# Kernel optimization log

Hardware: AMD Instinct MI355X
Metric: run time of the kernel (lower is better)

## Reference

```python
import jax, jax.numpy as jnp
import numpy as np

N = 50000      # nodes
E = 800000     # edges (before self-loops)
H = 2          # attention heads
C = 64         # hidden_channels (per-head out since concat=False)
L = 3          # num_layers - 2 conv blocks
OUT = 128      # readout out_channels
G = 512        # num graphs
VOCAB = 100    # embedding table size
NEG_SLOPE = 0.2


def setup_inputs() -> dict:
    key = jax.random.key(0)
    ks = jax.random.split(key, 12)
    s = 1.0 / np.sqrt(C)
    x = jax.random.randint(ks[0], (N,), 0, VOCAB, dtype=jnp.int32)
    edge_index = jax.random.randint(ks[1], (2, E), 0, N, dtype=jnp.int32)
    batch = jnp.sort(jax.random.randint(ks[2], (N,), 0, G, dtype=jnp.int32))
    embed = jax.random.normal(ks[3], (VOCAB, C), dtype=jnp.float32) * s
    lin_W = jax.random.normal(ks[4], (L, C, C), dtype=jnp.float32) * s
    lin_b = jnp.zeros((L, C), dtype=jnp.float32)
    gat_Wl = jax.random.normal(ks[5], (L, C, H * C), dtype=jnp.float32) * s
    gat_bl = jnp.zeros((L, H * C), dtype=jnp.float32)
    gat_Wr = jax.random.normal(ks[6], (L, C, H * C), dtype=jnp.float32) * s
    gat_br = jnp.zeros((L, H * C), dtype=jnp.float32)
    gat_att = jax.random.normal(ks[7], (L, H, C), dtype=jnp.float32) * s
    gat_bias = jnp.zeros((L, C), dtype=jnp.float32)
    readout_W = jax.random.normal(ks[8], (C, OUT), dtype=jnp.float32) * s
    readout_b = jnp.zeros((OUT,), dtype=jnp.float32)
    return {"x": x, "edge_index": edge_index, "batch": batch, "num_graphs": G,
            "embed": embed, "lin_W": lin_W, "lin_b": lin_b,
            "gat_Wl": gat_Wl, "gat_bl": gat_bl, "gat_Wr": gat_Wr, "gat_br": gat_br,
            "gat_att": gat_att, "gat_bias": gat_bias,
            "readout_W": readout_W, "readout_b": readout_b}


def _gatv2_layer(h, src, dst, Wl, bl, Wr, br, att, bias):
    # lin_l -> source/message features, lin_r -> target features (PyG GATv2Conv)
    xl = (h @ Wl + bl).reshape(N, H, C)
    xr = (h @ Wr + br).reshape(N, H, C)
    # per-edge GATv2 score: a^T LeakyReLU(x_l[j] + x_r[i])
    e = jax.nn.leaky_relu(xl[src] + xr[dst], NEG_SLOPE)      # [E2,H,C]
    score = jnp.einsum('ehc,hc->eh', e, att)                 # [E2,H]
    # segment softmax over incoming edges of each dst node (stable)
    m = jax.lax.stop_gradient(jax.ops.segment_max(score, dst, num_segments=N))
    p = jnp.exp(score - m[dst])
    denom = jax.ops.segment_sum(p, dst, num_segments=N)      # [N,H]
    alpha = p / denom[dst]                                   # [E2,H]
    msg = xl[src] * alpha[:, :, None]                        # [E2,H,C]
    agg = jax.ops.segment_sum(msg, dst, num_segments=N)      # [N,H,C]
    return agg.mean(axis=1) + bias                           # concat=False -> head mean


def reference(x, edge_index, batch, num_graphs, embed, lin_W, lin_b,
              gat_Wl, gat_bl, gat_Wr, gat_br, gat_att, gat_bias,
              readout_W, readout_b):
    # add self loops (GATv2Conv default add_self_loops=True)
    loops = jnp.arange(N, dtype=edge_index.dtype)
    src = jnp.concatenate([edge_index[0], loops])
    dst = jnp.concatenate([edge_index[1], loops])
    h = embed[x]                                             # [N,C]
    for l in range(L):
        h = jax.nn.relu(h @ lin_W[l] + lin_b[l])             # dropout is a no-op in eval
        h = _gatv2_layer(h, src, dst, gat_Wl[l], gat_bl[l], gat_Wr[l], gat_br[l],
                         gat_att[l], gat_bias[l])
    out = h @ readout_W + readout_b                          # [N,OUT]
    return jax.ops.segment_sum(out, batch, num_segments=num_graphs)  # [G,OUT]
```

## Files before the change

### kernel.cpp

```cpp
#include <hip/hip_runtime.h>
#include <hip/hip_fp16.h>

#define N_NODES  50000
#define E_EDGES  800000
#define E_TOT    850000
#define H_HEADS  2
#define C_DIM    64
#define HC       128
#define L_LAYERS 3
#define OUT_DIM  128
#define G_GRAPHS 512
#define NEG_SLOPE 0.2f
#define NB       196
#define EPB      4096

typedef float v2f __attribute__((ext_vector_type(2)));

__device__ __forceinline__ void lds_fence() { asm volatile("" ::: "memory"); }

__global__ void init_kernel(float* __restrict__ out, int* __restrict__ bucket_counts) {
    int i = blockIdx.x * 256 + threadIdx.x;
    if (i < G_GRAPHS * OUT_DIM) out[i] = 0.f;
    if (blockIdx.x == 0) bucket_counts[threadIdx.x] = 0;
}

__global__ void bucket_count_kernel(const int* __restrict__ dsts, int* __restrict__ bucket_counts) {
    __shared__ int hist[256];
    int tid = threadIdx.x;
    hist[tid] = 0;
    __syncthreads();
    int ebase = blockIdx.x * EPB;
#pragma unroll
    for (int i = 0; i < 16; i++) {
        int e = ebase + i * 256 + tid;
        if (e < E_TOT) {
            int d = (e < E_EDGES) ? dsts[e] : e - E_EDGES;
            atomicAdd(&hist[d >> 8], 1);
        }
    }
    __syncthreads();
    if (hist[tid]) atomicAdd(&bucket_counts[tid], hist[tid]);
}

__global__ void scan196_kernel(const int* __restrict__ bucket_counts,
                               int* __restrict__ bwptr, int* __restrict__ bbase) {
    __shared__ int wsum[4];
    int tid = threadIdx.x;
    int lane = tid & 63, wid = tid >> 6;
    int cnt = (tid < NB) ? bucket_counts[tid] : 0;
    int v = cnt;
#pragma unroll
    for (int off = 1; off < 64; off <<= 1) {
        int t = __shfl_up(v, off, 64);
        if (lane >= off) v += t;
    }
    if (lane == 63) wsum[wid] = v;
    __syncthreads();
    int woff = 0;
#pragma unroll
    for (int w = 0; w < 4; w++) if (w < wid) woff += wsum[w];
    v += woff;
    if (tid < NB) { bwptr[tid] = v - cnt; bbase[tid] = v - cnt; }
    if (tid == 0) bbase[NB] = E_TOT;
}

__global__ void edge_partition_kernel(const int* __restrict__ srcs, const int* __restrict__ dsts,
                                      int* __restrict__ bwptr, unsigned int* __restrict__ ebuf) {
    __shared__ int hist[256];
    __shared__ int lscan[256];
    __shared__ int sExcl[256];
    __shared__ int lcnt[256];
    __shared__ int gbase[256];
    __shared__ unsigned int sval[EPB];
    __shared__ unsigned char sgid[EPB];
    int tid = threadIdx.x;
    int ebase = blockIdx.x * EPB;
    hist[tid] = 0;
    __syncthreads();
    unsigned int val[16];
    int gid[16];
#pragma unroll
    for (int i = 0; i < 16; i++) {
        int e = ebase + i * 256 + tid;
        if (e < E_TOT) {
            int s, d;
            if (e < E_EDGES) { s = srcs[e]; d = dsts[e]; }
            else             { s = d = e - E_EDGES; }
            val[i] = ((unsigned)s << 8) | (unsigned)(d & 255);
            gid[i] = d >> 8;
            atomicAdd(&hist[gid[i]], 1);
        } else gid[i] = -1;
    }
    __syncthreads();
    lscan[tid] = hist[tid];
    __syncthreads();
#pragma unroll
    for (int off = 1; off < 256; off <<= 1) {
        int t = (tid >= off) ? lscan[tid - off] : 0;
        __syncthreads();
        lscan[tid] += t;
        __syncthreads();
    }
    sExcl[tid] = lscan[tid] - hist[tid];
    lcnt[tid] = 0;
    __syncthreads();
#pragma unroll
    for (int i = 0; i < 16; i++) {
        if (gid[i] >= 0) {
            int off = atomicAdd(&lcnt[gid[i]], 1);
            int idx = sExcl[gid[i]] + off;
            sval[idx] = val[i];
            sgid[idx] = (unsigned char)gid[i];
        }
    }
    if (tid < NB) {
        int c = hist[tid];
        gbase[tid] = c ? atomicAdd(&bwptr[tid], c) : 0;
    }
    __syncthreads();
    int total = lscan[255];
    for (int idx = tid; idx < total; idx += 256) {
        int g = sgid[idx];
        ebuf[gbase[g] + (idx - sExcl[g])] = sval[idx];
    }
}

__global__ void bucket_csr_kernel(const unsigned int* __restrict__ ebuf,
                                  const int* __restrict__ bbase,
                                  int* __restrict__ row_ptr,
                                  unsigned short* __restrict__ src_sorted) {
    __shared__ int hist[256];
    __shared__ int lcnt[256];
    __shared__ int wsum[4];
    int g = blockIdx.x, tid = threadIdx.x;
    int n0 = g << 8;
    int nodes = min(256, N_NODES - n0);
    int b0 = bbase[g], b1 = bbase[g + 1];
    int cnt = b1 - b0;
    hist[tid] = 0;
    lcnt[tid] = 0;
    __syncthreads();
    for (int i = tid; i < cnt; i += 256) atomicAdd(&hist[ebuf[b0 + i] & 255], 1);
    __syncthreads();
    int c = hist[tid];
    int v = c;
    int lane = tid & 63, wid = tid >> 6;
#pragma unroll
    for (int off = 1; off < 64; off <<= 1) {
        int t = __shfl_up(v, off, 64);
        if (lane >= off) v += t;
    }
    if (lane == 63) wsum[wid] = v;
    __syncthreads();
    int woff = 0;
#pragma unroll
    for (int w = 0; w < 4; w++) if (w < wid) woff += wsum[w];
    v += woff;
    int nbase = b0 + v - c;
    if (tid < nodes) row_ptr[n0 + tid] = nbase;
    if (g == NB - 1 && tid == 0) row_ptr[N_NODES] = E_TOT;
    __syncthreads();
    hist[tid] = nbase;
    __syncthreads();
    for (int i = tid; i < cnt; i += 256) {
        unsigned int e = ebuf[b0 + i];
        int dl = e & 255;
        int slot = hist[dl] + atomicAdd(&lcnt[dl], 1);
        src_sorted[slot] = (unsigned short)(e >> 8);
    }
}

__global__ void layer_lin_kernel(const float* __restrict__ h,
                                 const int* __restrict__ xs, const float* __restrict__ etab,
                                 int use_embed,
                                 const float* __restrict__ W, const float* __restrict__ b,
                                 const float* __restrict__ Wl, const float* __restrict__ bl,
                                 const float* __restrict__ Wr, const float* __restrict__ br,
                                 __half* __restrict__ xlh, float* __restrict__ xri) {
    __shared__ float sH[16 * 64];
    __shared__ float sH2[16 * 64];
    int tid = threadIdx.x;
    int base = blockIdx.x * 16;
#pragma unroll
    for (int i = 0; i < 4; i++) {
        int idx = tid + i * 256;
        int nn = base + (idx >> 6);
        int cc = idx & 63;
        float hv = 0.f;
        if (nn < N_NODES)
            hv = use_embed ? etab[xs[nn] * 64 + cc] : h[(size_t)nn * 64 + cc];
        sH[idx] = hv;
    }
    __syncthreads();
    {
        int c = tid & 63, g = tid >> 6;
        float a0 = b[c], a1 = a0, a2 = a0, a3 = a0;
        for (int k = 0; k < 64; k++) {
            float wv = W[k * 64 + c];
            a0 = fmaf(sH[(g * 4 + 0) * 64 + k], wv, a0);
            a1 = fmaf(sH[(g * 4 + 1) * 64 + k], wv, a1);
            a2 = fmaf(sH[(g * 4 + 2) * 64 + k], wv, a2);
            a3 = fmaf(sH[(g * 4 + 3) * 64 + k], wv, a3);
        }
        sH2[(g * 4 + 0) * 64 + c] = fmaxf(a0, 0.f);
        sH2[(g * 4 + 1) * 64 + c] = fmaxf(a1, 0.f);
        sH2[(g * 4 + 2) * 64 + c] = fmaxf(a2, 0.f);
        sH2[(g * 4 + 3) * 64 + c] = fmaxf(a3, 0.f);
    }
    __syncthreads();
    {
        int j = tid & 127, gg = tid >> 7;
        float accl[8], accr[8];
#pragma unroll
        for (int n = 0; n < 8; n++) { accl[n] = bl[j]; accr[n] = br[j]; }
        for (int k = 0; k < 64; k++) {
            float wl = Wl[k * 128 + j], wr = Wr[k * 128 + j];
#pragma unroll
            for (int n = 0; n < 8; n++) {
                float hv = sH2[(gg * 8 + n) * 64 + k];
                accl[n] = fmaf(hv, wl, accl[n]);
                accr[n] = fmaf(hv, wr, accr[n]);
            }
        }
        int hh = j >> 6, c = j & 63;
#pragma unroll
        for (int n = 0; n < 8; n++) {
            int node = base + gg * 8 + n;
            if (node < N_NODES) {
                size_t o = (size_t)node * 128 + c * 2 + hh;
                xlh[o] = __float2half(accl[n]);
                xri[o] = accr[n];
            }
        }
    }
}

__global__ void gat_kernel(const __half2* __restrict__ xlh, const float2* __restrict__ xr2,
                           const float* __restrict__ att, const int* __restrict__ row_ptr,
                           const unsigned short* __restrict__ src_sorted,
                           const float* __restrict__ bias,
                           float* __restrict__ h_out) {
    __shared__ __align__(16) float cbuf[4][8 * 132];
    int w = threadIdx.x >> 6;
    int d = blockIdx.x * 4 + w;
    if (d >= N_NODES) return;
    int lane = threadIdx.x & 63;
    int r0 = row_ptr[d], r1 = row_ptr[d + 1];
    float2 vrf = xr2[(size_t)d * 64 + lane];
    v2f vr2 = {vrf.x, vrf.y};
    v2f att2 = {att[lane], att[64 + lane]};
    float* cb = cbuf[w];
    int e_of = lane >> 3, p = lane & 7;

    float dpx = 0.f, dpy = 0.f;
    v2f ac0 = {0.f, 0.f}, ac1 = {0.f, 0.f};

#define GAT_LOAD(V, CB) do {                                                    \
        int lim_ = nchunk - 1;                                                  \
        _Pragma("unroll")                                                       \
        for (int e = 0; e < 8; e++) {                                           \
            int ee_ = (CB) + e;                                                 \
            int sv_ = __builtin_amdgcn_readlane(idx, (ee_ < nchunk) ? ee_ : lim_); \
            V[e] = xlh[(size_t)sv_ * 64 + lane];                                \
        }                                                                       \
    } while (0)

#define GAT_PROC(V, CB) do {                                                    \
        int rem_ = nchunk - (CB);                                               \
        v2f vf8[8];                                                             \
        _Pragma("unroll")                                                       \
        for (int e = 0; e < 8; e++) {                                           \
            float2 vf_ = __half22float2(V[e]);                                  \
            v2f vl2 = {vf_.x, vf_.y};                                           \
            vf8[e] = vl2;                                                       \
            v2f z = vl2 + vr2;                                                  \
            v2f t = __builtin_elementwise_max(z, z * NEG_SLOPE) * att2;         \
            *(v2f*)&cb[e * 132 + 2 * lane] = t;                                 \
        }                                                                       \
        lds_fence();                                                            \
        v2f s2 = {0.f, 0.f};                                                    \
        {                                                                       \
            const float4* row_ = (const float4*)&cb[e_of * 132 + p * 16];       \
            _Pragma("unroll")                                                   \
            for (int j = 0; j < 4; j++) {                                       \
                float4 f = row_[j];                                             \
                s2 += (v2f){f.x, f.y};                                          \
                s2 += (v2f){f.z, f.w};                                          \
            }                                                                   \
        }                                                                       \
        lds_fence();                                                            \
        _Pragma("unroll")                                                       \
        for (int off = 1; off <= 4; off <<= 1) {                                \
            v2f o_;                                                             \
            o_.x = __shfl_xor(s2.x, off, 64);                                   \
            o_.y = __shfl_xor(s2.y, off, 64);                                   \
            s2 += o_;                                                           \
        }                                                                       \
        float sx = s2.x, sy = s2.y;                                             \
        if (e_of >= rem_) { sx = -INFINITY; sy = -INFINITY; }                   \
        float wx = __expf(sx), wy = __expf(sy);                                 \
        dpx += wx; dpy += wy;                                                   \
        _Pragma("unroll")                                                       \
        for (int e = 0; e < 8; e++) {                                           \
            float swx = __int_as_float(__builtin_amdgcn_readlane(__float_as_int(wx), 8 * e)); \
            float swy = __int_as_float(__builtin_amdgcn_readlane(__float_as_int(wy), 8 * e)); \
            v2f w2 = {swx, swy};                                                \
            if (e & 1) ac1 = __builtin_elementwise_fma(w2, vf8[e], ac1);        \
            else       ac0 = __builtin_elementwise_fma(w2, vf8[e], ac0);        \
        }                                                                       \
    } while (0)

    for (int base = r0; base < r1; base += 64) {
        int a = base + lane;
        int idx = (int)src_sorted[(a < r1) ? a : (r1 - 1)];
        int nchunk = min(64, r1 - base);
        __half2 va[8], vb[8];
        GAT_LOAD(va, 0);
        int cb_i = 0;
        for (;;) {
            int nx = cb_i + 8;
            if (nx < nchunk) {
                GAT_LOAD(vb, nx);
                GAT_PROC(va, cb_i);
                cb_i = nx;
            } else {
                GAT_PROC(va, cb_i);
                break;
            }
            nx = cb_i + 8;
            if (nx < nchunk) {
                GAT_LOAD(va, nx);
                GAT_PROC(vb, cb_i);
                cb_i = nx;
            } else {
                GAT_PROC(vb, cb_i);
                break;
            }
        }
    }
#undef GAT_LOAD
#undef GAT_PROC

#pragma unroll
    for (int off = 8; off <= 32; off <<= 1) {
        dpx += __shfl_xor(dpx, off, 64);
        dpy += __shfl_xor(dpy, off, 64);
    }
    v2f acc = ac0 + ac1;
    h_out[(size_t)d * 64 + lane] = (acc.x / dpx + acc.y / dpy) * 0.5f + bias[lane];
}

__global__ void readout_kernel(const float* __restrict__ h, const float* __restrict__ W,
                               const float* __restrict__ b, const int* __restrict__ batch,
                               float* __restrict__ out) {
    __shared__ float sH[16 * 64];
    __shared__ int sB[16];
    int tid = threadIdx.x;
    int base = blockIdx.x * 16;
#pragma unroll
    for (int i = 0; i < 4; i++) {
        int idx = tid + i * 256;
        int nn = base + (idx >> 6);
        sH[idx] = (nn < N_NODES) ? h[(size_t)nn * 64 + (idx & 63)] : 0.f;
    }
    if (tid < 16) sB[tid] = (base + tid < N_NODES) ? batch[base + tid] : -1;
    __syncthreads();
    int j = tid & 127, gg = tid >> 7;
    float acc[8];
#pragma unroll
    for (int n = 0; n < 8; n++) acc[n] = b[j];
    for (int k = 0; k < 64; k++) {
        float wv = W[k * OUT_DIM + j];
#pragma unroll
        for (int n = 0; n < 8; n++) acc[n] = fmaf(sH[(gg * 8 + n) * 64 + k], wv, acc[n]);
    }
    float run = 0.f; int curb = -2;
#pragma unroll
    for (int n = 0; n < 8; n++) {
        int node = base + gg * 8 + n;
        int bb = (node < N_NODES) ? sB[gg * 8 + n] : -1;
        if (bb != curb) {
            if (curb >= 0) atomicAdd(&out[curb * OUT_DIM + j], run);
            run = 0.f; curb = bb;
        }
        if (bb >= 0) run += acc[n];
    }
    if (curb >= 0) atomicAdd(&out[curb * OUT_DIM + j], run);
}

extern "C" void kernel_launch(void* const* d_in, const int* in_sizes, int n_in,
                              void* d_out, int out_size, void* d_ws, size_t ws_size,
                              hipStream_t stream) {
    const int*   x        = (const int*)d_in[0];
    const int*   edge     = (const int*)d_in[1];
    const int*   batch    = (const int*)d_in[2];
    const float* embed    = (const float*)d_in[4];
    const float* lin_W    = (const float*)d_in[5];
    const float* lin_b    = (const float*)d_in[6];
    const float* gat_Wl   = (const float*)d_in[7];
    const float* gat_bl   = (const float*)d_in[8];
    const float* gat_Wr   = (const float*)d_in[9];
    const float* gat_br   = (const float*)d_in[10];
    const float* gat_att  = (const float*)d_in[11];
    const float* gat_bias = (const float*)d_in[12];
    const float* ro_W     = (const float*)d_in[13];
    const float* ro_b     = (const float*)d_in[14];
    float* out = (float*)d_out;

    const int* srcs = edge;
    const int* dsts = edge + E_EDGES;

    float* h    = (float*)d_ws;
    __half* xlh = (__half*)(h + (size_t)N_NODES * 64);
    float* xr   = (float*)((char*)xlh + (size_t)N_NODES * HC * sizeof(__half));
    int* row_ptr       = (int*)(xr + (size_t)N_NODES * HC);
    int* bwptr         = row_ptr + N_NODES + 1;
    int* bbase         = bwptr + 256;
    int* bucket_counts = bbase + 256;
    unsigned int* ebuf = (unsigned int*)(bucket_counts + 256);
    unsigned short* src_sorted = (unsigned short*)(ebuf + E_TOT);

    const int T = 256;
    const int gInit = (G_GRAPHS * OUT_DIM + 255) / 256;
    const int gPart = (E_TOT + EPB - 1) / EPB;
    const int gLin  = (N_NODES + 15) / 16;
    const int gGat  = (N_NODES + 3) / 4;

    init_kernel<<<gInit, T, 0, stream>>>(out, bucket_counts);
    bucket_count_kernel<<<gPart, T, 0, stream>>>(dsts, bucket_counts);
    scan196_kernel<<<1, T, 0, stream>>>(bucket_counts, bwptr, bbase);
    edge_partition_kernel<<<gPart, T, 0, stream>>>(srcs, dsts, bwptr, ebuf);
    bucket_csr_kernel<<<NB, T, 0, stream>>>(ebuf, bbase, row_ptr, src_sorted);

    for (int l = 0; l < L_LAYERS; l++) {
        layer_lin_kernel<<<gLin, T, 0, stream>>>(
            h, x, embed, (l == 0) ? 1 : 0,
            lin_W + (size_t)l * 64 * 64, lin_b + (size_t)l * 64,
            gat_Wl + (size_t)l * 64 * 128, gat_bl + (size_t)l * 128,
            gat_Wr + (size_t)l * 64 * 128, gat_br + (size_t)l * 128,
            xlh, xr);
        gat_kernel<<<gGat, T, 0, stream>>>(
            (const __half2*)xlh, (const float2*)xr, gat_att + (size_t)l * HC,
            row_ptr, src_sorted, gat_bias + (size_t)l * 64, h);
    }

    readout_kernel<<<gLin, T, 0, stream>>>(h, ro_W, ro_b, batch, out);
}
```

Measured before the change: 407.8 us.

## Store xr in fp16, transpose LDS tiles with packed FMA, shrink GAT blocks

Three separate changes. xr is now stored as fp16 instead of fp32, which halves its write and read traffic. The linear and readout kernels now keep transposed LDS tiles, so float4 LDS reads feed packed v2f FMAs. The GAT kernel runs 128-thread blocks (two waves) instead of 256, which is meant to give finer scheduling granularity. The fp16 xr lowers precision of the attention score inputs.

```diff
diff --git a/kernel.cpp b/kernel.cpp
--- a/kernel.cpp
+++ b/kernel.cpp
@@ -176,9 +176,9 @@
                                  const float* __restrict__ W, const float* __restrict__ b,
                                  const float* __restrict__ Wl, const float* __restrict__ bl,
                                  const float* __restrict__ Wr, const float* __restrict__ br,
-                                 __half* __restrict__ xlh, float* __restrict__ xri) {
-    __shared__ float sH[16 * 64];
-    __shared__ float sH2[16 * 64];
+                                 __half* __restrict__ xlh, __half* __restrict__ xrh) {
+    __shared__ float sHT[64 * 16];
+    __shared__ float sH2T[64 * 16];
     int tid = threadIdx.x;
     int base = blockIdx.x * 16;
 #pragma unroll
@@ -189,64 +189,75 @@
         float hv = 0.f;
         if (nn < N_NODES)
             hv = use_embed ? etab[xs[nn] * 64 + cc] : h[(size_t)nn * 64 + cc];
-        sH[idx] = hv;
+        sHT[cc * 16 + (idx >> 6)] = hv;
     }
     __syncthreads();
     {
         int c = tid & 63, g = tid >> 6;
-        float a0 = b[c], a1 = a0, a2 = a0, a3 = a0;
+        v2f a01 = {b[c], b[c]}, a23 = a01;
         for (int k = 0; k < 64; k++) {
             float wv = W[k * 64 + c];
-            a0 = fmaf(sH[(g * 4 + 0) * 64 + k], wv, a0);
-            a1 = fmaf(sH[(g * 4 + 1) * 64 + k], wv, a1);
-            a2 = fmaf(sH[(g * 4 + 2) * 64 + k], wv, a2);
-            a3 = fmaf(sH[(g * 4 + 3) * 64 + k], wv, a3);
-        }
-        sH2[(g * 4 + 0) * 64 + c] = fmaxf(a0, 0.f);
-        sH2[(g * 4 + 1) * 64 + c] = fmaxf(a1, 0.f);
-        sH2[(g * 4 + 2) * 64 + c] = fmaxf(a2, 0.f);
-        sH2[(g * 4 + 3) * 64 + c] = fmaxf(a3, 0.f);
+            v2f w2 = {wv, wv};
+            float4 hA = *(const float4*)&sHT[k * 16 + g * 4];
+            a01 = __builtin_elementwise_fma((v2f){hA.x, hA.y}, w2, a01);
+            a23 = __builtin_elementwise_fma((v2f){hA.z, hA.w}, w2, a23);
+        }
+        float4 r;
+        r.x = fmaxf(a01.x, 0.f); r.y = fmaxf(a01.y, 0.f);
+        r.z = fmaxf(a23.x, 0.f); r.w = fmaxf(a23.y, 0.f);
+        *(float4*)&sH2T[c * 16 + g * 4] = r;
     }
     __syncthreads();
     {
         int j = tid & 127, gg = tid >> 7;
-        float accl[8], accr[8];
-#pragma unroll
-        for (int n = 0; n < 8; n++) { accl[n] = bl[j]; accr[n] = br[j]; }
+        v2f accl2[4], accr2[4];
+#pragma unroll
+        for (int m = 0; m < 4; m++) { accl2[m] = (v2f){bl[j], bl[j]}; accr2[m] = (v2f){br[j], br[j]}; }
         for (int k = 0; k < 64; k++) {
             float wl = Wl[k * 128 + j], wr = Wr[k * 128 + j];
-#pragma unroll
-            for (int n = 0; n < 8; n++) {
-                float hv = sH2[(gg * 8 + n) * 64 + k];
-                accl[n] = fmaf(hv, wl, accl[n]);
-                accr[n] = fmaf(hv, wr, accr[n]);
+            v2f wl2 = {wl, wl}, wr2 = {wr, wr};
+            float4 hA = *(const float4*)&sH2T[k * 16 + gg * 8];
+            float4 hB = *(const float4*)&sH2T[k * 16 + gg * 8 + 4];
+            accl2[0] = __builtin_elementwise_fma((v2f){hA.x, hA.y}, wl2, accl2[0]);
+            accl2[1] = __builtin_elementwise_fma((v2f){hA.z, hA.w}, wl2, accl2[1]);
+            accl2[2] = __builtin_elementwise_fma((v2f){hB.x, hB.y}, wl2, accl2[2]);
+            accl2[3] = __builtin_elementwise_fma((v2f){hB.z, hB.w}, wl2, accl2[3]);
+            accr2[0] = __builtin_elementwise_fma((v2f){hA.x, hA.y}, wr2, accr2[0]);
+            accr2[1] = __builtin_elementwise_fma((v2f){hA.z, hA.w}, wr2, accr2[1]);
+            accr2[2] = __builtin_elementwise_fma((v2f){hB.x, hB.y}, wr2, accr2[2]);
+            accr2[3] = __builtin_elementwise_fma((v2f){hB.z, hB.w}, wr2, accr2[3]);
+        }
+        int hh = j >> 6, c = j & 63;
+#pragma unroll
+        for (int m = 0; m < 4; m++) {
+#pragma unroll
+            for (int s = 0; s < 2; s++) {
+                int node = base + gg * 8 + 2 * m + s;
+                if (node < N_NODES) {
+                    size_t o = (size_t)node * 128 + c * 2 + hh;
+                    float vl = s ? accl2[m].y : accl2[m].x;
+                    float vr = s ? accr2[m].y : accr2[m].x;
+                    xlh[o] = __float2half(vl);
+                    xrh[o] = __float2half(vr);
+                }
             }
         }
-        int hh = j >> 6, c = j & 63;
-#pragma unroll
-        for (int n = 0; n < 8; n++) {
-            int node = base + gg * 8 + n;
-            if (node < N_NODES) {
-                size_t o = (size_t)node * 128 + c * 2 + hh;
-                xlh[o] = __float2half(accl[n]);
-                xri[o] = accr[n];
-            }
-        }
-    }
-}
-
-__global__ void gat_kernel(const __half2* __restrict__ xlh, const float2* __restrict__ xr2,
-                           const float* __restrict__ att, const int* __restrict__ row_ptr,
-                           const unsigned short* __restrict__ src_sorted,
-                           const float* __restrict__ bias,
-                           float* __restrict__ h_out) {
-    __shared__ __align__(16) float cbuf[4][8 * 132];
+    }
+}
+
+__global__ void __launch_bounds__(128)
+gat_kernel(const __half2* __restrict__ xlh, const __half2* __restrict__ xrh2,
+           const float* __restrict__ att, const int* __restrict__ row_ptr,
+           const unsigned short* __restrict__ src_sorted,
+           const float* __restrict__ bias,
+           float* __restrict__ h_out) {
+    __shared__ __align__(16) float cbuf[2][8 * 132];
     int w = threadIdx.x >> 6;
-    int d = blockIdx.x * 4 + w;
+    int d = blockIdx.x * 2 + w;
     if (d >= N_NODES) return;
     int lane = threadIdx.x & 63;
     int r0 = row_ptr[d], r1 = row_ptr[d + 1];
-    float2 vrf = xr2[(size_t)d * 64 + lane];
+    float2 vrf = __half22float2(xrh2[(size_t)d * 64 + lane]);
     v2f vr2 = {vrf.x, vrf.y};
     v2f att2 = {att[lane], att[64 + lane]};
     float* cb = cbuf[w];
@@ -353,7 +364,7 @@
 __global__ void readout_kernel(const float* __restrict__ h, const float* __restrict__ W,
                                const float* __restrict__ b, const int* __restrict__ batch,
                                float* __restrict__ out) {
-    __shared__ float sH[16 * 64];
+    __shared__ float sHT[64 * 16];
     __shared__ int sB[16];
     int tid = threadIdx.x;
     int base = blockIdx.x * 16;
@@ -361,29 +372,36 @@
     for (int i = 0; i < 4; i++) {
         int idx = tid + i * 256;
         int nn = base + (idx >> 6);
-        sH[idx] = (nn < N_NODES) ? h[(size_t)nn * 64 + (idx & 63)] : 0.f;
+        float hv = (nn < N_NODES) ? h[(size_t)nn * 64 + (idx & 63)] : 0.f;
+        sHT[(idx & 63) * 16 + (idx >> 6)] = hv;
     }
     if (tid < 16) sB[tid] = (base + tid < N_NODES) ? batch[base + tid] : -1;
     __syncthreads();
     int j = tid & 127, gg = tid >> 7;
-    float acc[8];
-#pragma unroll
-    for (int n = 0; n < 8; n++) acc[n] = b[j];
+    v2f acc2[4];
+#pragma unroll
+    for (int m = 0; m < 4; m++) acc2[m] = (v2f){b[j], b[j]};
     for (int k = 0; k < 64; k++) {
         float wv = W[k * OUT_DIM + j];
-#pragma unroll
-        for (int n = 0; n < 8; n++) acc[n] = fmaf(sH[(gg * 8 + n) * 64 + k], wv, acc[n]);
+        v2f w2 = {wv, wv};
+        float4 hA = *(const float4*)&sHT[k * 16 + gg * 8];
+        float4 hB = *(const float4*)&sHT[k * 16 + gg * 8 + 4];
+        acc2[0] = __builtin_elementwise_fma((v2f){hA.x, hA.y}, w2, acc2[0]);
+        acc2[1] = __builtin_elementwise_fma((v2f){hA.z, hA.w}, w2, acc2[1]);
+        acc2[2] = __builtin_elementwise_fma((v2f){hB.x, hB.y}, w2, acc2[2]);
+        acc2[3] = __builtin_elementwise_fma((v2f){hB.z, hB.w}, w2, acc2[3]);
     }
     float run = 0.f; int curb = -2;
 #pragma unroll
     for (int n = 0; n < 8; n++) {
         int node = base + gg * 8 + n;
         int bb = (node < N_NODES) ? sB[gg * 8 + n] : -1;
+        float av = (n & 1) ? acc2[n >> 1].y : acc2[n >> 1].x;
         if (bb != curb) {
             if (curb >= 0) atomicAdd(&out[curb * OUT_DIM + j], run);
             run = 0.f; curb = bb;
         }
-        if (bb >= 0) run += acc[n];
+        if (bb >= 0) run += av;
     }
     if (curb >= 0) atomicAdd(&out[curb * OUT_DIM + j], run);
 }
@@ -412,8 +430,8 @@
 
     float* h    = (float*)d_ws;
     __half* xlh = (__half*)(h + (size_t)N_NODES * 64);
-    float* xr   = (float*)((char*)xlh + (size_t)N_NODES * HC * sizeof(__half));
-    int* row_ptr       = (int*)(xr + (size_t)N_NODES * HC);
+    __half* xrh = xlh + (size_t)N_NODES * HC;
+    int* row_ptr       = (int*)(xrh + (size_t)N_NODES * HC);
     int* bwptr         = row_ptr + N_NODES + 1;
     int* bbase         = bwptr + 256;
     int* bucket_counts = bbase + 256;
@@ -424,7 +442,7 @@
     const int gInit = (G_GRAPHS * OUT_DIM + 255) / 256;
     const int gPart = (E_TOT + EPB - 1) / EPB;
     const int gLin  = (N_NODES + 15) / 16;
-    const int gGat  = (N_NODES + 3) / 4;
+    const int gGat  = (N_NODES + 1) / 2;
 
     init_kernel<<<gInit, T, 0, stream>>>(out, bucket_counts);
     bucket_count_kernel<<<gPart, T, 0, stream>>>(dsts, bucket_counts);
@@ -438,9 +456,9 @@
             lin_W + (size_t)l * 64 * 64, lin_b + (size_t)l * 64,
             gat_Wl + (size_t)l * 64 * 128, gat_bl + (size_t)l * 128,
             gat_Wr + (size_t)l * 64 * 128, gat_br + (size_t)l * 128,
-            xlh, xr);
-        gat_kernel<<<gGat, T, 0, stream>>>(
-            (const __half2*)xlh, (const float2*)xr, gat_att + (size_t)l * HC,
+            xlh, xrh);
+        gat_kernel<<<gGat, 128, 0, stream>>>(
+            (const __half2*)xlh, (const __half2*)xrh, gat_att + (size_t)l * HC,
             row_ptr, src_sorted, gat_bias + (size_t)l * 64, h);
     }
 
```

Result: slower. 1.491 ms (+265.6%).

## Fuse CSR build into cooperative kernel, store xr in fp16, shrink GAT blocks

Applied to the files above, without the earlier changes.

Folds the five CSR-construction kernels (init, bucket count, scan, partition, per-bucket CSR) into one cooperative kernel on 256 blocks, separated by grid-wide syncs, to cut launch overhead and inter-kernel gaps. The target-side projection xr is now stored as fp16 instead of fp32, halving its write and read traffic in the linear and GAT kernels. The GAT kernel moves from 256-thread to 128-thread blocks (two destination nodes per block) for finer scheduling. Risks are the cost of grid.sync and fewer blocks during CSR build, plus reduced precision in the attention logits.

```diff
diff --git a/kernel.cpp b/kernel.cpp
--- a/kernel.cpp
+++ b/kernel.cpp
@@ -1,5 +1,8 @@
 #include <hip/hip_runtime.h>
 #include <hip/hip_fp16.h>
+#include <hip/hip_cooperative_groups.h>
+
+namespace cg = cooperative_groups;
 
 #define N_NODES  50000
 #define E_EDGES  800000
@@ -13,59 +16,19 @@
 #define NEG_SLOPE 0.2f
 #define NB       196
 #define EPB      4096
+#define NCHUNK   ((E_TOT + EPB - 1) / EPB)
 
 typedef float v2f __attribute__((ext_vector_type(2)));
 
 __device__ __forceinline__ void lds_fence() { asm volatile("" ::: "memory"); }
 
-__global__ void init_kernel(float* __restrict__ out, int* __restrict__ bucket_counts) {
-    int i = blockIdx.x * 256 + threadIdx.x;
-    if (i < G_GRAPHS * OUT_DIM) out[i] = 0.f;
-    if (blockIdx.x == 0) bucket_counts[threadIdx.x] = 0;
-}
-
-__global__ void bucket_count_kernel(const int* __restrict__ dsts, int* __restrict__ bucket_counts) {
-    __shared__ int hist[256];
-    int tid = threadIdx.x;
-    hist[tid] = 0;
-    __syncthreads();
-    int ebase = blockIdx.x * EPB;
-#pragma unroll
-    for (int i = 0; i < 16; i++) {
-        int e = ebase + i * 256 + tid;
-        if (e < E_TOT) {
-            int d = (e < E_EDGES) ? dsts[e] : e - E_EDGES;
-            atomicAdd(&hist[d >> 8], 1);
-        }
-    }
-    __syncthreads();
-    if (hist[tid]) atomicAdd(&bucket_counts[tid], hist[tid]);
-}
-
-__global__ void scan196_kernel(const int* __restrict__ bucket_counts,
-                               int* __restrict__ bwptr, int* __restrict__ bbase) {
-    __shared__ int wsum[4];
-    int tid = threadIdx.x;
-    int lane = tid & 63, wid = tid >> 6;
-    int cnt = (tid < NB) ? bucket_counts[tid] : 0;
-    int v = cnt;
-#pragma unroll
-    for (int off = 1; off < 64; off <<= 1) {
-        int t = __shfl_up(v, off, 64);
-        if (lane >= off) v += t;
-    }
-    if (lane == 63) wsum[wid] = v;
-    __syncthreads();
-    int woff = 0;
-#pragma unroll
-    for (int w = 0; w < 4; w++) if (w < wid) woff += wsum[w];
-    v += woff;
-    if (tid < NB) { bwptr[tid] = v - cnt; bbase[tid] = v - cnt; }
-    if (tid == 0) bbase[NB] = E_TOT;
-}
-
-__global__ void edge_partition_kernel(const int* __restrict__ srcs, const int* __restrict__ dsts,
-                                      int* __restrict__ bwptr, unsigned int* __restrict__ ebuf) {
+__global__ void __launch_bounds__(256)
+csr_fused_kernel(const int* __restrict__ srcs, const int* __restrict__ dsts,
+                 float* __restrict__ out, int* __restrict__ bucket_counts,
+                 int* __restrict__ bwptr, int* __restrict__ bbase,
+                 int* __restrict__ row_ptr, unsigned int* __restrict__ ebuf,
+                 unsigned short* __restrict__ src_sorted) {
+    cg::grid_group grid = cg::this_grid();
     __shared__ int hist[256];
     __shared__ int lscan[256];
     __shared__ int sExcl[256];
@@ -74,99 +37,142 @@
     __shared__ unsigned int sval[EPB];
     __shared__ unsigned char sgid[EPB];
     int tid = threadIdx.x;
-    int ebase = blockIdx.x * EPB;
-    hist[tid] = 0;
-    __syncthreads();
-    unsigned int val[16];
-    int gid[16];
-#pragma unroll
-    for (int i = 0; i < 16; i++) {
-        int e = ebase + i * 256 + tid;
-        if (e < E_TOT) {
-            int s, d;
-            if (e < E_EDGES) { s = srcs[e]; d = dsts[e]; }
-            else             { s = d = e - E_EDGES; }
-            val[i] = ((unsigned)s << 8) | (unsigned)(d & 255);
-            gid[i] = d >> 8;
-            atomicAdd(&hist[gid[i]], 1);
-        } else gid[i] = -1;
-    }
-    __syncthreads();
-    lscan[tid] = hist[tid];
-    __syncthreads();
-#pragma unroll
-    for (int off = 1; off < 256; off <<= 1) {
-        int t = (tid >= off) ? lscan[tid - off] : 0;
-        __syncthreads();
-        lscan[tid] += t;
-        __syncthreads();
-    }
-    sExcl[tid] = lscan[tid] - hist[tid];
-    lcnt[tid] = 0;
-    __syncthreads();
-#pragma unroll
-    for (int i = 0; i < 16; i++) {
-        if (gid[i] >= 0) {
-            int off = atomicAdd(&lcnt[gid[i]], 1);
-            int idx = sExcl[gid[i]] + off;
-            sval[idx] = val[i];
-            sgid[idx] = (unsigned char)gid[i];
-        }
-    }
-    if (tid < NB) {
+    int bid = blockIdx.x;
+    int nb = gridDim.x;
+
+    for (int i = bid * 256 + tid; i < G_GRAPHS * OUT_DIM; i += nb * 256) out[i] = 0.f;
+    if (bid == 0) bucket_counts[tid] = 0;
+    grid.sync();
+
+    for (int c = bid; c < NCHUNK; c += nb) {
+        hist[tid] = 0;
+        __syncthreads();
+        int ebase = c * EPB;
+#pragma unroll
+        for (int i = 0; i < 16; i++) {
+            int e = ebase + i * 256 + tid;
+            if (e < E_TOT) {
+                int d = (e < E_EDGES) ? dsts[e] : e - E_EDGES;
+                atomicAdd(&hist[d >> 8], 1);
+            }
+        }
+        __syncthreads();
+        if (hist[tid]) atomicAdd(&bucket_counts[tid], hist[tid]);
+        __syncthreads();
+    }
+    grid.sync();
+
+    if (bid == 0) {
+        int lane = tid & 63, wid = tid >> 6;
+        int cnt = (tid < NB) ? bucket_counts[tid] : 0;
+        int v = cnt;
+#pragma unroll
+        for (int off = 1; off < 64; off <<= 1) {
+            int t = __shfl_up(v, off, 64);
+            if (lane >= off) v += t;
+        }
+        if (lane == 63) gbase[wid] = v;
+        __syncthreads();
+        int woff = 0;
+#pragma unroll
+        for (int w = 0; w < 4; w++) if (w < wid) woff += gbase[w];
+        v += woff;
+        if (tid < NB) { bwptr[tid] = v - cnt; bbase[tid] = v - cnt; }
+        if (tid == 0) bbase[NB] = E_TOT;
+    }
+    grid.sync();
+
+    for (int c = bid; c < NCHUNK; c += nb) {
+        int ebase = c * EPB;
+        hist[tid] = 0;
+        __syncthreads();
+        unsigned int val[16];
+        int gid[16];
+#pragma unroll
+        for (int i = 0; i < 16; i++) {
+            int e = ebase + i * 256 + tid;
+            if (e < E_TOT) {
+                int s, d;
+                if (e < E_EDGES) { s = srcs[e]; d = dsts[e]; }
+                else             { s = d = e - E_EDGES; }
+                val[i] = ((unsigned)s << 8) | (unsigned)(d & 255);
+                gid[i] = d >> 8;
+                atomicAdd(&hist[gid[i]], 1);
+            } else gid[i] = -1;
+        }
+        __syncthreads();
+        lscan[tid] = hist[tid];
+        __syncthreads();
+#pragma unroll
+        for (int off = 1; off < 256; off <<= 1) {
+            int t = (tid >= off) ? lscan[tid - off] : 0;
+            __syncthreads();
+            lscan[tid] += t;
+            __syncthreads();
+        }
+        sExcl[tid] = lscan[tid] - hist[tid];
+        lcnt[tid] = 0;
+        __syncthreads();
+#pragma unroll
+        for (int i = 0; i < 16; i++) {
+            if (gid[i] >= 0) {
+                int off = atomicAdd(&lcnt[gid[i]], 1);
+                int idx = sExcl[gid[i]] + off;
+                sval[idx] = val[i];
+                sgid[idx] = (unsigned char)gid[i];
+            }
+        }
+        if (tid < NB) {
+            int cc = hist[tid];
+            gbase[tid] = cc ? atomicAdd(&bwptr[tid], cc) : 0;
+        }
+        __syncthreads();
+        int total = lscan[255];
+        for (int idx = tid; idx < total; idx += 256) {
+            int g = sgid[idx];
+            ebuf[gbase[g] + (idx - sExcl[g])] = sval[idx];
+        }
+        __syncthreads();
+    }
+    grid.sync();
+
+    for (int g = bid; g < NB; g += nb) {
+        int n0 = g << 8;
+        int nodes = min(256, N_NODES - n0);
+        int b0 = bbase[g], b1 = bbase[g + 1];
+        int cnt = b1 - b0;
+        hist[tid] = 0;
+        lcnt[tid] = 0;
+        __syncthreads();
+        for (int i = tid; i < cnt; i += 256) atomicAdd(&hist[ebuf[b0 + i] & 255], 1);
+        __syncthreads();
         int c = hist[tid];
-        gbase[tid] = c ? atomicAdd(&bwptr[tid], c) : 0;
-    }
-    __syncthreads();
-    int total = lscan[255];
-    for (int idx = tid; idx < total; idx += 256) {
-        int g = sgid[idx];
-        ebuf[gbase[g] + (idx - sExcl[g])] = sval[idx];
-    }
-}
-
-__global__ void bucket_csr_kernel(const unsigned int* __restrict__ ebuf,
-                                  const int* __restrict__ bbase,
-                                  int* __restrict__ row_ptr,
-                                  unsigned short* __restrict__ src_sorted) {
-    __shared__ int hist[256];
-    __shared__ int lcnt[256];
-    __shared__ int wsum[4];
-    int g = blockIdx.x, tid = threadIdx.x;
-    int n0 = g << 8;
-    int nodes = min(256, N_NODES - n0);
-    int b0 = bbase[g], b1 = bbase[g + 1];
-    int cnt = b1 - b0;
-    hist[tid] = 0;
-    lcnt[tid] = 0;
-    __syncthreads();
-    for (int i = tid; i < cnt; i += 256) atomicAdd(&hist[ebuf[b0 + i] & 255], 1);
-    __syncthreads();
-    int c = hist[tid];
-    int v = c;
-    int lane = tid & 63, wid = tid >> 6;
-#pragma unroll
-    for (int off = 1; off < 64; off <<= 1) {
-        int t = __shfl_up(v, off, 64);
-        if (lane >= off) v += t;
-    }
-    if (lane == 63) wsum[wid] = v;
-    __syncthreads();
-    int woff = 0;
-#pragma unroll
-    for (int w = 0; w < 4; w++) if (w < wid) woff += wsum[w];
-    v += woff;
-    int nbase = b0 + v - c;
-    if (tid < nodes) row_ptr[n0 + tid] = nbase;
-    if (g == NB - 1 && tid == 0) row_ptr[N_NODES] = E_TOT;
-    __syncthreads();
-    hist[tid] = nbase;
-    __syncthreads();
-    for (int i = tid; i < cnt; i += 256) {
-        unsigned int e = ebuf[b0 + i];
-        int dl = e & 255;
-        int slot = hist[dl] + atomicAdd(&lcnt[dl], 1);
-        src_sorted[slot] = (unsigned short)(e >> 8);
+        int v = c;
+        int lane = tid & 63, wid = tid >> 6;
+#pragma unroll
+        for (int off = 1; off < 64; off <<= 1) {
+            int t = __shfl_up(v, off, 64);
+            if (lane >= off) v += t;
+        }
+        if (lane == 63) lscan[wid] = v;
+        __syncthreads();
+        int woff = 0;
+#pragma unroll
+        for (int w = 0; w < 4; w++) if (w < wid) woff += lscan[w];
+        v += woff;
+        int nbase = b0 + v - c;
+        if (tid < nodes) row_ptr[n0 + tid] = nbase;
+        if (g == NB - 1 && tid == 0) row_ptr[N_NODES] = E_TOT;
+        __syncthreads();
+        hist[tid] = nbase;
+        __syncthreads();
+        for (int i = tid; i < cnt; i += 256) {
+            unsigned int e = ebuf[b0 + i];
+            int dl = e & 255;
+            int slot = hist[dl] + atomicAdd(&lcnt[dl], 1);
+            src_sorted[slot] = (unsigned short)(e >> 8);
+        }
+        __syncthreads();
     }
 }
 
@@ -176,7 +182,7 @@
                                  const float* __restrict__ W, const float* __restrict__ b,
                                  const float* __restrict__ Wl, const float* __restrict__ bl,
                                  const float* __restrict__ Wr, const float* __restrict__ br,
-                                 __half* __restrict__ xlh, float* __restrict__ xri) {
+                                 __half* __restrict__ xlh, __half* __restrict__ xrh) {
     __shared__ float sH[16 * 64];
     __shared__ float sH2[16 * 64];
     int tid = threadIdx.x;
@@ -229,24 +235,25 @@
             if (node < N_NODES) {
                 size_t o = (size_t)node * 128 + c * 2 + hh;
                 xlh[o] = __float2half(accl[n]);
-                xri[o] = accr[n];
+                xrh[o] = __float2half(accr[n]);
             }
         }
     }
 }
 
-__global__ void gat_kernel(const __half2* __restrict__ xlh, const float2* __restrict__ xr2,
-                           const float* __restrict__ att, const int* __restrict__ row_ptr,
-                           const unsigned short* __restrict__ src_sorted,
-                           const float* __restrict__ bias,
-                           float* __restrict__ h_out) {
-    __shared__ __align__(16) float cbuf[4][8 * 132];
+__global__ void __launch_bounds__(128)
+gat_kernel(const __half2* __restrict__ xlh, const __half2* __restrict__ xrh2,
+           const float* __restrict__ att, const int* __restrict__ row_ptr,
+           const unsigned short* __restrict__ src_sorted,
+           const float* __restrict__ bias,
+           float* __restrict__ h_out) {
+    __shared__ __align__(16) float cbuf[2][8 * 132];
     int w = threadIdx.x >> 6;
-    int d = blockIdx.x * 4 + w;
+    int d = blockIdx.x * 2 + w;
     if (d >= N_NODES) return;
     int lane = threadIdx.x & 63;
     int r0 = row_ptr[d], r1 = row_ptr[d + 1];
-    float2 vrf = xr2[(size_t)d * 64 + lane];
+    float2 vrf = __half22float2(xrh2[(size_t)d * 64 + lane]);
     v2f vr2 = {vrf.x, vrf.y};
     v2f att2 = {att[lane], att[64 + lane]};
     float* cb = cbuf[w];
@@ -412,8 +419,8 @@
 
     float* h    = (float*)d_ws;
     __half* xlh = (__half*)(h + (size_t)N_NODES * 64);
-    float* xr   = (float*)((char*)xlh + (size_t)N_NODES * HC * sizeof(__half));
-    int* row_ptr       = (int*)(xr + (size_t)N_NODES * HC);
+    __half* xrh = xlh + (size_t)N_NODES * HC;
+    int* row_ptr       = (int*)(xrh + (size_t)N_NODES * HC);
     int* bwptr         = row_ptr + N_NODES + 1;
     int* bbase         = bwptr + 256;
     int* bucket_counts = bbase + 256;
@@ -421,16 +428,16 @@
     unsigned short* src_sorted = (unsigned short*)(ebuf + E_TOT);
 
     const int T = 256;
-    const int gInit = (G_GRAPHS * OUT_DIM + 255) / 256;
-    const int gPart = (E_TOT + EPB - 1) / EPB;
-    const int gLin  = (N_NODES + 15) / 16;
-    const int gGat  = (N_NODES + 3) / 4;
-
-    init_kernel<<<gInit, T, 0, stream>>>(out, bucket_counts);
-    bucket_count_kernel<<<gPart, T, 0, stream>>>(dsts, bucket_counts);
-    scan196_kernel<<<1, T, 0, stream>>>(bucket_counts, bwptr, bbase);
-    edge_partition_kernel<<<gPart, T, 0, stream>>>(srcs, dsts, bwptr, ebuf);
-    bucket_csr_kernel<<<NB, T, 0, stream>>>(ebuf, bbase, row_ptr, src_sorted);
+    const int gLin = (N_NODES + 15) / 16;
+    const int gGat = (N_NODES + 1) / 2;
+
+    {
+        void* args[] = {(void*)&srcs, (void*)&dsts, (void*)&out, (void*)&bucket_counts,
+                        (void*)&bwptr, (void*)&bbase, (void*)&row_ptr, (void*)&ebuf,
+                        (void*)&src_sorted};
+        hipLaunchCooperativeKernel((const void*)csr_fused_kernel,
+                                   dim3(256), dim3(T), args, 0, stream);
+    }
 
     for (int l = 0; l < L_LAYERS; l++) {
         layer_lin_kernel<<<gLin, T, 0, stream>>>(
@@ -438,9 +445,9 @@
             lin_W + (size_t)l * 64 * 64, lin_b + (size_t)l * 64,
             gat_Wl + (size_t)l * 64 * 128, gat_bl + (size_t)l * 128,
             gat_Wr + (size_t)l * 64 * 128, gat_br + (size_t)l * 128,
-            xlh, xr);
-        gat_kernel<<<gGat, T, 0, stream>>>(
-            (const __half2*)xlh, (const float2*)xr, gat_att + (size_t)l * HC,
+            xlh, xrh);
+        gat_kernel<<<gGat, 128, 0, stream>>>(
+            (const __half2*)xlh, (const __half2*)xrh, gat_att + (size_t)l * HC,
             row_ptr, src_sorted, gat_bias + (size_t)l * 64, h);
     }
 
```

Measured after the change: 532.9 us. 1.31x slower.

## Drop bucket count/scan pass with fixed-stride buckets, store xr as fp16, shrink GAT blocks

Applied to the files above, without the earlier changes.

The separate bucket histogram and scan kernels are removed. Edges are now written into fixed-stride per-bucket slots (BSTRIDE = 4864) using the running atomic counters, and each node gets a (start,end) pair instead of a row_ptr array. The target features xr are stored in half precision to cut write and read traffic, and the GAT kernel now runs two nodes per 128-thread block. This saves two launches and one pass over the edges, but it assumes no bucket ever exceeds the fixed stride, which holds for random uniform destinations and lowers precision on xr.

```diff
diff --git a/kernel.cpp b/kernel.cpp
--- a/kernel.cpp
+++ b/kernel.cpp
@@ -13,55 +13,16 @@
 #define NEG_SLOPE 0.2f
 #define NB       196
 #define EPB      4096
+#define BSTRIDE  4864
 
 typedef float v2f __attribute__((ext_vector_type(2)));
 
 __device__ __forceinline__ void lds_fence() { asm volatile("" ::: "memory"); }
 
-__global__ void init_kernel(float* __restrict__ out, int* __restrict__ bucket_counts) {
+__global__ void init_kernel(float* __restrict__ out, int* __restrict__ bwptr) {
     int i = blockIdx.x * 256 + threadIdx.x;
     if (i < G_GRAPHS * OUT_DIM) out[i] = 0.f;
-    if (blockIdx.x == 0) bucket_counts[threadIdx.x] = 0;
-}
-
-__global__ void bucket_count_kernel(const int* __restrict__ dsts, int* __restrict__ bucket_counts) {
-    __shared__ int hist[256];
-    int tid = threadIdx.x;
-    hist[tid] = 0;
-    __syncthreads();
-    int ebase = blockIdx.x * EPB;
-#pragma unroll
-    for (int i = 0; i < 16; i++) {
-        int e = ebase + i * 256 + tid;
-        if (e < E_TOT) {
-            int d = (e < E_EDGES) ? dsts[e] : e - E_EDGES;
-            atomicAdd(&hist[d >> 8], 1);
-        }
-    }
-    __syncthreads();
-    if (hist[tid]) atomicAdd(&bucket_counts[tid], hist[tid]);
-}
-
-__global__ void scan196_kernel(const int* __restrict__ bucket_counts,
-                               int* __restrict__ bwptr, int* __restrict__ bbase) {
-    __shared__ int wsum[4];
-    int tid = threadIdx.x;
-    int lane = tid & 63, wid = tid >> 6;
-    int cnt = (tid < NB) ? bucket_counts[tid] : 0;
-    int v = cnt;
-#pragma unroll
-    for (int off = 1; off < 64; off <<= 1) {
-        int t = __shfl_up(v, off, 64);
-        if (lane >= off) v += t;
-    }
-    if (lane == 63) wsum[wid] = v;
-    __syncthreads();
-    int woff = 0;
-#pragma unroll
-    for (int w = 0; w < 4; w++) if (w < wid) woff += wsum[w];
-    v += woff;
-    if (tid < NB) { bwptr[tid] = v - cnt; bbase[tid] = v - cnt; }
-    if (tid == 0) bbase[NB] = E_TOT;
+    if (blockIdx.x == 0) bwptr[threadIdx.x] = 0;
 }
 
 __global__ void edge_partition_kernel(const int* __restrict__ srcs, const int* __restrict__ dsts,
@@ -121,13 +82,13 @@
     int total = lscan[255];
     for (int idx = tid; idx < total; idx += 256) {
         int g = sgid[idx];
-        ebuf[gbase[g] + (idx - sExcl[g])] = sval[idx];
+        ebuf[(size_t)g * BSTRIDE + gbase[g] + (idx - sExcl[g])] = sval[idx];
     }
 }
 
 __global__ void bucket_csr_kernel(const unsigned int* __restrict__ ebuf,
-                                  const int* __restrict__ bbase,
-                                  int* __restrict__ row_ptr,
+                                  const int* __restrict__ bwptr,
+                                  int2* __restrict__ row_se,
                                   unsigned short* __restrict__ src_sorted) {
     __shared__ int hist[256];
     __shared__ int lcnt[256];
@@ -135,8 +96,8 @@
     int g = blockIdx.x, tid = threadIdx.x;
     int n0 = g << 8;
     int nodes = min(256, N_NODES - n0);
-    int b0 = bbase[g], b1 = bbase[g + 1];
-    int cnt = b1 - b0;
+    int b0 = g * BSTRIDE;
+    int cnt = bwptr[g];
     hist[tid] = 0;
     lcnt[tid] = 0;
     __syncthreads();
@@ -157,8 +118,7 @@
     for (int w = 0; w < 4; w++) if (w < wid) woff += wsum[w];
     v += woff;
     int nbase = b0 + v - c;
-    if (tid < nodes) row_ptr[n0 + tid] = nbase;
-    if (g == NB - 1 && tid == 0) row_ptr[N_NODES] = E_TOT;
+    if (tid < nodes) row_se[n0 + tid] = make_int2(nbase, nbase + c);
     __syncthreads();
     hist[tid] = nbase;
     __syncthreads();
@@ -176,7 +136,7 @@
                                  const float* __restrict__ W, const float* __restrict__ b,
                                  const float* __restrict__ Wl, const float* __restrict__ bl,
                                  const float* __restrict__ Wr, const float* __restrict__ br,
-                                 __half* __restrict__ xlh, float* __restrict__ xri) {
+                                 __half* __restrict__ xlh, __half* __restrict__ xrh) {
     __shared__ float sH[16 * 64];
     __shared__ float sH2[16 * 64];
     int tid = threadIdx.x;
@@ -229,24 +189,26 @@
             if (node < N_NODES) {
                 size_t o = (size_t)node * 128 + c * 2 + hh;
                 xlh[o] = __float2half(accl[n]);
-                xri[o] = accr[n];
+                xrh[o] = __float2half(accr[n]);
             }
         }
     }
 }
 
-__global__ void gat_kernel(const __half2* __restrict__ xlh, const float2* __restrict__ xr2,
-                           const float* __restrict__ att, const int* __restrict__ row_ptr,
-                           const unsigned short* __restrict__ src_sorted,
-                           const float* __restrict__ bias,
-                           float* __restrict__ h_out) {
-    __shared__ __align__(16) float cbuf[4][8 * 132];
+__global__ void __launch_bounds__(128)
+gat_kernel(const __half2* __restrict__ xlh, const __half2* __restrict__ xrh2,
+           const float* __restrict__ att, const int2* __restrict__ row_se,
+           const unsigned short* __restrict__ src_sorted,
+           const float* __restrict__ bias,
+           float* __restrict__ h_out) {
+    __shared__ __align__(16) float cbuf[2][8 * 132];
     int w = threadIdx.x >> 6;
-    int d = blockIdx.x * 4 + w;
+    int d = blockIdx.x * 2 + w;
     if (d >= N_NODES) return;
     int lane = threadIdx.x & 63;
-    int r0 = row_ptr[d], r1 = row_ptr[d + 1];
-    float2 vrf = xr2[(size_t)d * 64 + lane];
+    int2 se = row_se[d];
+    int r0 = se.x, r1 = se.y;
+    float2 vrf = __half22float2(xrh2[(size_t)d * 64 + lane]);
     v2f vr2 = {vrf.x, vrf.y};
     v2f att2 = {att[lane], att[64 + lane]};
     float* cb = cbuf[w];
@@ -412,25 +374,21 @@
 
     float* h    = (float*)d_ws;
     __half* xlh = (__half*)(h + (size_t)N_NODES * 64);
-    float* xr   = (float*)((char*)xlh + (size_t)N_NODES * HC * sizeof(__half));
-    int* row_ptr       = (int*)(xr + (size_t)N_NODES * HC);
-    int* bwptr         = row_ptr + N_NODES + 1;
-    int* bbase         = bwptr + 256;
-    int* bucket_counts = bbase + 256;
-    unsigned int* ebuf = (unsigned int*)(bucket_counts + 256);
-    unsigned short* src_sorted = (unsigned short*)(ebuf + E_TOT);
+    __half* xrh = xlh + (size_t)N_NODES * HC;
+    int2* row_se       = (int2*)(xrh + (size_t)N_NODES * HC);
+    int* bwptr         = (int*)(row_se + N_NODES);
+    unsigned int* ebuf = (unsigned int*)(bwptr + 256);
+    unsigned short* src_sorted = (unsigned short*)(ebuf + (size_t)NB * BSTRIDE);
 
     const int T = 256;
     const int gInit = (G_GRAPHS * OUT_DIM + 255) / 256;
     const int gPart = (E_TOT + EPB - 1) / EPB;
     const int gLin  = (N_NODES + 15) / 16;
-    const int gGat  = (N_NODES + 3) / 4;
-
-    init_kernel<<<gInit, T, 0, stream>>>(out, bucket_counts);
-    bucket_count_kernel<<<gPart, T, 0, stream>>>(dsts, bucket_counts);
-    scan196_kernel<<<1, T, 0, stream>>>(bucket_counts, bwptr, bbase);
+    const int gGat  = (N_NODES + 1) / 2;
+
+    init_kernel<<<gInit, T, 0, stream>>>(out, bwptr);
     edge_partition_kernel<<<gPart, T, 0, stream>>>(srcs, dsts, bwptr, ebuf);
-    bucket_csr_kernel<<<NB, T, 0, stream>>>(ebuf, bbase, row_ptr, src_sorted);
+    bucket_csr_kernel<<<NB, T, 0, stream>>>(ebuf, bwptr, row_se, src_sorted);
 
     for (int l = 0; l < L_LAYERS; l++) {
         layer_lin_kernel<<<gLin, T, 0, stream>>>(
@@ -438,10 +396,10 @@
             lin_W + (size_t)l * 64 * 64, lin_b + (size_t)l * 64,
             gat_Wl + (size_t)l * 64 * 128, gat_bl + (size_t)l * 128,
             gat_Wr + (size_t)l * 64 * 128, gat_br + (size_t)l * 128,
-            xlh, xr);
-        gat_kernel<<<gGat, T, 0, stream>>>(
-            (const __half2*)xlh, (const float2*)xr, gat_att + (size_t)l * HC,
-            row_ptr, src_sorted, gat_bias + (size_t)l * 64, h);
+            xlh, xrh);
+        gat_kernel<<<gGat, 128, 0, stream>>>(
+            (const __half2*)xlh, (const __half2*)xrh, gat_att + (size_t)l * HC,
+            row_se, src_sorted, gat_bias + (size_t)l * 64, h);
     }
 
     readout_kernel<<<gLin, T, 0, stream>>>(h, ro_W, ro_b, batch, out);
```

Measured after the change: 399.9 us. Within noise of the previous version (-2.0%).
